# Optimization experiments

Measured on AMD Instinct MI355X. Metric: run time of the kernel, lower is better.

The kernel has to match this reference:

```python
import jax, jax.numpy as jnp
import numpy as np

B, N, T = 16, 1024, 100
SPEED = 0.05  # diffusion_speed


def make_Qt():
    # Qt[t-1] = [[1-p, p], [p, 1-p]], p = 0.5*(1 - (1-2*speed)^t), t in [1, T]
    ts = jnp.arange(1, T + 1, dtype=jnp.float32)
    flip = 0.5 * (1.0 - (1.0 - 2.0 * SPEED) ** ts)
    nf = 1.0 - flip
    return jnp.stack([jnp.stack([nf, flip], -1), jnp.stack([flip, nf], -1)], -2)  # [T,2,2]


def setup_inputs() -> dict:
    key = jax.random.key(0)
    k1, k2, k3 = jax.random.split(key, 3)
    adj_start = jax.random.randint(k1, (B, N, N), 0, 2, dtype=jnp.int32)
    t = jax.random.randint(k2, (B,), 0, T, dtype=jnp.int32)
    # denoise_fn output stand-in: per-edge Bernoulli probs in (0,1)
    q_approx = jax.random.uniform(k3, (B * N * N,), dtype=jnp.float32, minval=1e-4, maxval=1.0 - 1e-4)
    return {"adj_start": adj_start, "t": t, "q_approx": q_approx, "Qt": make_Qt()}


def reference(adj_start, t, q_approx, Qt):
    b = adj_start.shape[0]
    bidx = jnp.arange(b)[:, None, None]                      # [B,1,1]

    # ---- forward_diffusion: q = Qt[t][adj_start]; adj_t ~ Categorical(q) ----
    Q_ev = Qt[t]                                             # [B,2,2]
    q_fwd = Q_ev[bidx, adj_start]                            # [B,N,N,2]
    adj_t = jax.random.categorical(jax.random.key(42), jnp.log(q_fwd), axis=-1).astype(jnp.int32)

    # ---- backward_diffusion: posterior q(x_{t-1} | x_t, x_0) ----
    likelihood = Qt[0][adj_t]                                # [B,N,N,2]
    prior = Qt[t - 1][bidx, adj_start]                       # [B,N,N,2]
    evidence = Q_ev[bidx, adj_start, adj_t]                  # [B,N,N]
    q_backward = likelihood * prior / evidence[..., None]    # [B,N,N,2]
    q_target = q_backward[..., 0].reshape(-1)                # [B*N*N]

    # ---- loss: BCE(q_approx, q_target), torch-style log clamping ----
    logp = jnp.clip(jnp.log(q_approx), -100.0)
    log1mp = jnp.clip(jnp.log1p(-q_approx), -100.0)
    loss = -jnp.mean(q_target * logp + (1.0 - q_target) * log1mp)
    return loss
```

## Files before the change

kernel.cpp:

```cpp
#include <hip/hip_runtime.h>
#include <stdint.h>


#define T_STEPS 100
#define NE 16777216
#define EPT 16
#define NBLK (NE / EPT / 256)

struct BTab {
  uint32_t thr0, thr1;
  float qt00, qt01, qt10, qt11;
};

__device__ __forceinline__ BTab make_tab(const float* __restrict__ Qt, int tb) {
  int tm1 = (tb == 0) ? (T_STEPS - 1) : (tb - 1);
  float e00 = Qt[tb * 4 + 0], e01 = Qt[tb * 4 + 1];
  float e10 = Qt[tb * 4 + 2], e11 = Qt[tb * 4 + 3];
  float p0 = Qt[tm1 * 4 + 0];
  float p1 = Qt[tm1 * 4 + 2];
  float L00 = Qt[0];
  float L10 = Qt[2];
  BTab t;
  t.thr0 = (uint32_t)((double)e01 * 4294967296.0);
  t.thr1 = (uint32_t)((double)e11 * 4294967296.0);
  t.qt00 = L00 * p0 / e00;
  t.qt01 = L10 * p0 / e01;
  t.qt10 = L00 * p1 / e10;
  t.qt11 = L10 * p1 / e11;
  return t;
}

__device__ __forceinline__ uint32_t chash(uint32_t e) {
  uint32_t h = e * 0x9E3779B1u;
  h ^= h >> 16;
  h *= 0x85EBCA6Bu;
  return h;
}

__device__ __forceinline__ float elem_term(uint32_t e, int a, const BTab& bt,
                                           float q) {
  uint32_t thr = a ? bt.thr1 : bt.thr0;
  bool adj1 = chash(e) < thr;
  float qt = a ? (adj1 ? bt.qt11 : bt.qt10)
               : (adj1 ? bt.qt01 : bt.qt00);
  float logp  = __logf(q);
  float log1m = __logf(1.0f - q);
  return fmaf(qt, logp - log1m, log1m);
}

__global__ __launch_bounds__(256, 8) void diff_loss_kernel(
    const int* __restrict__ adj, const int* __restrict__ tvec,
    const float* __restrict__ qap, const float* __restrict__ Qt,
    double* __restrict__ ws) {
  const int tid = blockIdx.x * 256 + threadIdx.x;
  const uint32_t e0 = (uint32_t)tid * EPT;
  const int b = blockIdx.x >> 8;
  const BTab bt = make_tab(Qt, tvec[b]);

  const int4*   a4 = (const int4*)(adj + e0);
  const float4* q4 = (const float4*)(qap + e0);
  int4   aV[4];
  float4 qV[4];
#pragma unroll
  for (int i = 0; i < 4; ++i) aV[i] = a4[i];
#pragma unroll
  for (int i = 0; i < 4; ++i) qV[i] = q4[i];
  __builtin_amdgcn_sched_barrier(0);

  float s = 0.0f;
#pragma unroll
  for (int i = 0; i < 4; ++i) {
    uint32_t eb = e0 + 4u * (uint32_t)i;
    s += elem_term(eb + 0u, aV[i].x, bt, qV[i].x);
    s += elem_term(eb + 1u, aV[i].y, bt, qV[i].y);
    s += elem_term(eb + 2u, aV[i].z, bt, qV[i].z);
    s += elem_term(eb + 3u, aV[i].w, bt, qV[i].w);
  }

#pragma unroll
  for (int off = 32; off > 0; off >>= 1)
    s += __shfl_down(s, off, 64);

  __shared__ float red[4];
  const int lane = threadIdx.x & 63;
  const int wv = threadIdx.x >> 6;
  if (lane == 0) red[wv] = s;
  __syncthreads();
  if (threadIdx.x == 0)
    ws[blockIdx.x] = (double)red[0] + (double)red[1] +
                     (double)red[2] + (double)red[3];
}

__global__ __launch_bounds__(256) void finalize_k(
    const double* __restrict__ ws, float* __restrict__ out) {
  double s = 0.0;
  const int base = threadIdx.x * 16;
#pragma unroll
  for (int i = 0; i < 16; ++i) s += ws[base + i];
#pragma unroll
  for (int off = 32; off > 0; off >>= 1)
    s += __shfl_down(s, off, 64);
  __shared__ double red[4];
  const int lane = threadIdx.x & 63;
  const int wv = threadIdx.x >> 6;
  if (lane == 0) red[wv] = s;
  __syncthreads();
  if (threadIdx.x == 0) {
    double tot = red[0] + red[1] + red[2] + red[3];
    out[0] = (float)(-tot / (double)NE);
  }
}

extern "C" void kernel_launch(void* const* d_in, const int* in_sizes, int n_in,
                              void* d_out, int out_size, void* d_ws, size_t ws_size,
                              hipStream_t stream) {
  const int*   adj = (const int*)d_in[0];
  const int*   tv  = (const int*)d_in[1];
  const float* qap = (const float*)d_in[2];
  const float* Qt  = (const float*)d_in[3];
  double* ws = (double*)d_ws;

  diff_loss_kernel<<<NBLK, 256, 0, stream>>>(adj, tv, qap, Qt, ws);
  finalize_k<<<1, 256, 0, stream>>>(ws, (float*)d_out);
}
```

Before: 156.9 us.

## Use block-strided coalesced loads with software prefetch in loss kernel

Reorganizes work so each block covers 8192 contiguous elements and each thread walks it in 1024-element strides, giving fully coalesced 16-byte loads per wave instruction. Adds a two-deep register prefetch pipeline and halves the grid to 2048 blocks, with finalize adjusted to sum 2048 partials. Aims to improve memory access efficiency and overlap loads with log computation, at the cost of fewer outstanding loads per thread than the previous up-front batch.

```diff
diff --git a/kernel.cpp b/kernel.cpp
--- a/kernel.cpp
+++ b/kernel.cpp
@@ -4,8 +4,8 @@
 
 #define T_STEPS 100
 #define NE 16777216
-#define EPT 16
-#define NBLK (NE / EPT / 256)
+#define NBLK 2048
+#define IPT 8
 
 struct BTab {
   uint32_t thr0, thr1;
@@ -48,33 +48,36 @@
   return fmaf(qt, logp - log1m, log1m);
 }
 
-__global__ __launch_bounds__(256, 8) void diff_loss_kernel(
+__global__ __launch_bounds__(256, 4) void diff_loss_kernel(
     const int* __restrict__ adj, const int* __restrict__ tvec,
     const float* __restrict__ qap, const float* __restrict__ Qt,
     double* __restrict__ ws) {
-  const int tid = blockIdx.x * 256 + threadIdx.x;
-  const uint32_t e0 = (uint32_t)tid * EPT;
-  const int b = blockIdx.x >> 8;
+  const int b = blockIdx.x >> 7;
   const BTab bt = make_tab(Qt, tvec[b]);
+  const uint32_t base =
+      (uint32_t)blockIdx.x * 8192u + (uint32_t)threadIdx.x * 4u;
 
-  const int4*   a4 = (const int4*)(adj + e0);
-  const float4* q4 = (const float4*)(qap + e0);
-  int4   aV[4];
-  float4 qV[4];
-#pragma unroll
-  for (int i = 0; i < 4; ++i) aV[i] = a4[i];
-#pragma unroll
-  for (int i = 0; i < 4; ++i) qV[i] = q4[i];
-  __builtin_amdgcn_sched_barrier(0);
+  int4   a0 = *(const int4*)(adj + base);
+  float4 q0 = *(const float4*)(qap + base);
+  int4   a1 = *(const int4*)(adj + base + 1024u);
+  float4 q1 = *(const float4*)(qap + base + 1024u);
 
   float s = 0.0f;
 #pragma unroll
-  for (int i = 0; i < 4; ++i) {
-    uint32_t eb = e0 + 4u * (uint32_t)i;
-    s += elem_term(eb + 0u, aV[i].x, bt, qV[i].x);
-    s += elem_term(eb + 1u, aV[i].y, bt, qV[i].y);
-    s += elem_term(eb + 2u, aV[i].z, bt, qV[i].z);
-    s += elem_term(eb + 3u, aV[i].w, bt, qV[i].w);
+  for (int i = 0; i < IPT; ++i) {
+    int4 an = a1; float4 qn = q1;
+    if (i + 2 < IPT) {
+      const uint32_t ep = base + (uint32_t)(i + 2) * 1024u;
+      an = *(const int4*)(adj + ep);
+      qn = *(const float4*)(qap + ep);
+    }
+    const uint32_t e = base + (uint32_t)i * 1024u;
+    s += elem_term(e + 0u, a0.x, bt, q0.x);
+    s += elem_term(e + 1u, a0.y, bt, q0.y);
+    s += elem_term(e + 2u, a0.z, bt, q0.z);
+    s += elem_term(e + 3u, a0.w, bt, q0.w);
+    a0 = a1; q0 = q1;
+    a1 = an; q1 = qn;
   }
 
 #pragma unroll
@@ -94,9 +97,9 @@
 __global__ __launch_bounds__(256) void finalize_k(
     const double* __restrict__ ws, float* __restrict__ out) {
   double s = 0.0;
-  const int base = threadIdx.x * 16;
+  const int base = threadIdx.x * 8;
 #pragma unroll
-  for (int i = 0; i < 16; ++i) s += ws[base + i];
+  for (int i = 0; i < 8; ++i) s += ws[base + i];
 #pragma unroll
   for (int off = 32; off > 0; off >>= 1)
     s += __shfl_down(s, off, 64);
```

Result: slower. 161.2 us (+2.8%).
